# Kernel optimization log

Hardware: AMD Instinct MI355X
Metric: run time of the kernel (lower is better)

Reference implementation:

```python
import jax, jax.numpy as jnp
import numpy as np

N_OBJECTS = 32  # mask labels 1..32 (0 = background)


def setup_inputs() -> dict:
    key = jax.random.key(0)
    k1, k2, k3, k4 = jax.random.split(key, 4)
    B, F, H, W = 8, 64, 256, 256
    encoded = jax.random.normal(k1, (B, F, H, W), dtype=jnp.float32)
    masks = jax.random.randint(k2, (B, 1, H, W), 0, N_OBJECTS + 1, dtype=jnp.int32)
    W1 = jax.random.normal(k3, (2 * F, F // 2), dtype=jnp.float32) * 0.05
    b1 = jnp.zeros((F // 2,), dtype=jnp.float32)
    W2 = jax.random.normal(k4, (F // 2, 4), dtype=jnp.float32) * 0.05
    b2 = jnp.zeros((4,), dtype=jnp.float32)
    return {"encoded": encoded, "masks": masks, "W1": W1, "b1": b1, "W2": W2, "b2": b2}


def reference(encoded, masks, W1, b1, W2, b2):
    B, F, H, W = encoded.shape
    # --- masked per-object max-pool (segment max over pixels) ---
    enc = encoded.reshape(B, F, H * W).transpose(0, 2, 1)  # [B, HW, F]
    ids = masks.reshape(B, H * W)                          # [B, HW]
    seg_max = jax.vmap(
        lambda d, i: jax.ops.segment_max(d, i, num_segments=N_OBJECTS + 1)
    )(enc, ids)                                            # [B, N+1, F]
    vectors = seg_max[:, 1:, :]                            # [B, N, F] (skip label 0)

    # --- O(N^2) pairwise MLP: connections[b,c,j,i] = sigmoid(MLP([v_i; v_j])) ---
    N = vectors.shape[1]
    vi = jnp.broadcast_to(vectors[:, :, None, :], (B, N, N, F))  # v_i over axis 1
    vj = jnp.broadcast_to(vectors[:, None, :, :], (B, N, N, F))  # v_j over axis 2
    pairs = jnp.concatenate([vi, vj], axis=-1)                   # [B, N, N, 2F]
    h = jnp.einsum('bijd,dh->bijh', pairs, W1) + b1
    out = jax.nn.sigmoid(jnp.einsum('bijh,hc->bijc', h, W2) + b2)  # [B, Ni, Nj, C]
    connections = out.transpose(0, 3, 2, 1)                        # [B, C, Nj, Ni]
    return vectors, connections
```

## Files before the change

### kernel.cpp

```cpp
#include <hip/hip_runtime.h>
#include <math.h>

#define B_      8
#define F_      64
#define HW_     65536
#define NSEG    33
#define NOBJ    32
#define FPB     8
#define SLICES  16
#define PIXB    (HW_ / SLICES)
#define ENC_NEG_INF 0x007FFFFFu

__device__ __forceinline__ unsigned enc_f(float x) {
    unsigned u = __float_as_uint(x);
    return u ^ ((unsigned)((int)u >> 31) | 0x80000000u);
}
__device__ __forceinline__ float dec_f(unsigned e) {
    unsigned x = (e & 0x80000000u) ? (e ^ 0x80000000u) : ~e;
    return __uint_as_float(x);
}


__global__ __launch_bounds__(256) void segmax_kernel(
        const float* __restrict__ enc, const int* __restrict__ masks,
        float* __restrict__ part) {
    __shared__ unsigned acc[FPB * NSEG * 32];
    const int tid = threadIdx.x;
    const int blk = blockIdx.x;
    const int b     = blk >> 7;
    const int fg    = (blk >> 4) & 7;
    const int slice = blk & 15;

    for (int i = tid; i < FPB * NSEG * 32; i += 256) acc[i] = ENC_NEG_INF;
    __syncthreads();

    const int fl = tid >> 5;
    const int l  = tid & 31;
    unsigned* a = acc + fl * (NSEG * 32) + l;

    const float4* ep = (const float4*)(enc + ((size_t)(b * F_ + fg * FPB + fl)) * HW_
                                       + slice * PIXB) + l;
    const int4*   mp = (const int4*)(masks + (size_t)b * HW_ + slice * PIXB) + l;

    #pragma unroll 8
    for (int c = 0; c < PIXB / 128; ++c) {
        float4 v  = ep[c * 32];
        int4   id = mp[c * 32];
        atomicMax(a + id.x * 32, enc_f(v.x));
        atomicMax(a + id.y * 32, enc_f(v.y));
        atomicMax(a + id.z * 32, enc_f(v.z));
        atomicMax(a + id.w * 32, enc_f(v.w));
    }
    __syncthreads();

    float* dst = part + (((size_t)b * SLICES + slice) * NSEG) * F_;
    for (int cell = tid; cell < FPB * NSEG; cell += 256) {
        int f = cell & 7, s = cell >> 3;
        const unsigned* row = acc + f * (NSEG * 32) + s * 32;
        unsigned m = ENC_NEG_INF;
        #pragma unroll
        for (int k = 0; k < 32; k += 4) {
            uint4 q = *(const uint4*)(row + k);
            unsigned m1 = q.x > q.y ? q.x : q.y;
            unsigned m2 = q.z > q.w ? q.z : q.w;
            unsigned m3 = m1 > m2 ? m1 : m2;
            m = m > m3 ? m : m3;
        }
        dst[s * F_ + fg * FPB + f] = dec_f(m);
    }
}

__global__ __launch_bounds__(256) void mlp_kernel(
        const float* __restrict__ part,
        const float* __restrict__ W1, const float* __restrict__ b1,
        const float* __restrict__ W2, const float* __restrict__ b2,
        float* __restrict__ out_vec, float* __restrict__ out_conn) {
    const int b   = blockIdx.x >> 2;
    const int it  = blockIdx.x & 3;
    const int tid = threadIdx.x;
    __shared__ float v[NOBJ * 65];
    __shared__ float w1s[2 * F_ * 32];
    __shared__ float w2s[32 * 4];
    __shared__ float b1s[32];
    __shared__ float Am[8 * 36];
    __shared__ float Bm[NOBJ * 36];

    for (int i = tid; i < 2 * F_ * 32 / 4; i += 256)
        ((float4*)w1s)[i] = ((const float4*)W1)[i];
    if (tid < 32) { w2s[tid*4+0]=W2[tid*4+0]; w2s[tid*4+1]=W2[tid*4+1];
                    w2s[tid*4+2]=W2[tid*4+2]; w2s[tid*4+3]=W2[tid*4+3];
                    b1s[tid] = b1[tid]; }

    for (int cell = tid; cell < NOBJ * F_; cell += 256) {
        int s = (cell >> 6) + 1, f = cell & 63;
        float m = -INFINITY;
        #pragma unroll
        for (int sl = 0; sl < SLICES; ++sl)
            m = fmaxf(m, part[(((size_t)b * SLICES + sl) * NSEG + s) * F_ + f]);
        v[(s - 1) * 65 + f] = m;
        if (it == 0) out_vec[b * NOBJ * F_ + cell] = m;
    }
    __syncthreads();

    for (int d = tid; d < 320; d += 256) {
        int kg, obj, half;
        if (d < 64) { half = 0; obj = it * 8 + (d >> 3); kg = d & 7; }
        else        { half = 1; obj = (d - 64) >> 3;     kg = d & 7; }
        const float* vv = v + obj * 65;
        const float* w  = w1s + half * (F_ * 32) + kg * 4;
        float4 s4 = {0.f, 0.f, 0.f, 0.f};
        #pragma unroll
        for (int f = 0; f < F_; ++f) {
            float4 wf = *(const float4*)(w + f * 32);
            float x = vv[f];
            s4.x = fmaf(x, wf.x, s4.x); s4.y = fmaf(x, wf.y, s4.y);
            s4.z = fmaf(x, wf.z, s4.z); s4.w = fmaf(x, wf.w, s4.w);
        }
        if (half == 0) {
            float4 bb = *(const float4*)(b1s + kg * 4);
            s4.x += bb.x; s4.y += bb.y; s4.z += bb.z; s4.w += bb.w;
            *(float4*)(Am + (d >> 3) * 36 + kg * 4) = s4;
        } else {
            *(float4*)(Bm + obj * 36 + kg * 4) = s4;
        }
    }
    __syncthreads();

    {
        int i_loc = tid >> 5, j = tid & 31;
        float o0 = b2[0], o1 = b2[1], o2 = b2[2], o3 = b2[3];
        #pragma unroll
        for (int kg = 0; kg < 8; ++kg) {
            float4 ha = *(const float4*)(Am + i_loc * 36 + kg * 4);
            float4 hb = *(const float4*)(Bm + j * 36 + kg * 4);
            float h0 = ha.x + hb.x, h1 = ha.y + hb.y;
            float h2 = ha.z + hb.z, h3 = ha.w + hb.w;
            const float* w2 = w2s + kg * 16;
            o0 = fmaf(h0, w2[0],  fmaf(h1, w2[4],  fmaf(h2, w2[8],  fmaf(h3, w2[12], o0))));
            o1 = fmaf(h0, w2[1],  fmaf(h1, w2[5],  fmaf(h2, w2[9],  fmaf(h3, w2[13], o1))));
            o2 = fmaf(h0, w2[2],  fmaf(h1, w2[6],  fmaf(h2, w2[10], fmaf(h3, w2[14], o2))));
            o3 = fmaf(h0, w2[3],  fmaf(h1, w2[7],  fmaf(h2, w2[11], fmaf(h3, w2[15], o3))));
        }
        float* oc = out_conn + (size_t)b * 4 * NOBJ * NOBJ + j * NOBJ + (it * 8 + i_loc);
        oc[0 * NOBJ * NOBJ] = 1.f / (1.f + expf(-o0));
        oc[1 * NOBJ * NOBJ] = 1.f / (1.f + expf(-o1));
        oc[2 * NOBJ * NOBJ] = 1.f / (1.f + expf(-o2));
        oc[3 * NOBJ * NOBJ] = 1.f / (1.f + expf(-o3));
    }
}

extern "C" void kernel_launch(void* const* d_in, const int* in_sizes, int n_in,
                              void* d_out, int out_size, void* d_ws, size_t ws_size,
                              hipStream_t stream) {
    const float* enc   = (const float*)d_in[0];
    const int*   masks = (const int*)  d_in[1];
    const float* W1    = (const float*)d_in[2];
    const float* b1    = (const float*)d_in[3];
    const float* W2    = (const float*)d_in[4];
    const float* b2    = (const float*)d_in[5];

    float* out_vec  = (float*)d_out;
    float* out_conn = out_vec + B_ * NOBJ * F_;
    float* part     = (float*)d_ws;

    segmax_kernel<<<B_ * (F_ / FPB) * SLICES, 256, 0, stream>>>(enc, masks, part);
    mlp_kernel<<<B_ * 4, 256, 0, stream>>>(part, W1, b1, W2, b2, out_vec, out_conn);
}
```

Baseline: 217.1 us.

## Merge slice partials via global atomicMax and batch loads before LDS atomics

Instead of writing 16 per-slice partial maxima and reducing them in the MLP kernel, each segmax block folds its result into a pre-initialised global buffer with a guarded atomicMax, and the MLP kernel just decodes one value per cell. The segment-0 background row is no longer reduced or stored. The main loop now issues 8 vector loads before the LDS atomics so more memory requests are in flight, and the launch bounds ask for 4 blocks per CU. This adds a third small kernel launch for initialisation and global atomic traffic, in exchange for removing the partial-buffer reduction and giving the load-bound pixel loop more memory-level parallelism.

```diff
diff --git a/kernel.cpp b/kernel.cpp
--- a/kernel.cpp
+++ b/kernel.cpp
@@ -7,6 +7,7 @@
 #define NSEG    33
 #define NOBJ    32
 #define FPB     8
+#define FGRP    (F_ / FPB)
 #define SLICES  16
 #define PIXB    (HW_ / SLICES)
 #define ENC_NEG_INF 0x007FFFFFu
@@ -20,16 +21,18 @@
     return __uint_as_float(x);
 }
 
+__global__ void init_ws(unsigned* __restrict__ gws) {
+    gws[blockIdx.x * blockDim.x + threadIdx.x] = ENC_NEG_INF;
+}
 
-__global__ __launch_bounds__(256) void segmax_kernel(
+__global__ __launch_bounds__(256, 4) void segmax_kernel(
         const float* __restrict__ enc, const int* __restrict__ masks,
-        float* __restrict__ part) {
+        unsigned* __restrict__ gws) {
     __shared__ unsigned acc[FPB * NSEG * 32];
-    const int tid = threadIdx.x;
-    const int blk = blockIdx.x;
-    const int b     = blk >> 7;
-    const int fg    = (blk >> 4) & 7;
-    const int slice = blk & 15;
+    const int tid   = threadIdx.x;
+    const int b     = blockIdx.x >> 7;
+    const int fg    = (blockIdx.x >> 4) & 7;
+    const int slice = blockIdx.x & 15;
 
     for (int i = tid; i < FPB * NSEG * 32; i += 256) acc[i] = ENC_NEG_INF;
     __syncthreads();
@@ -42,36 +45,41 @@
                                        + slice * PIXB) + l;
     const int4*   mp = (const int4*)(masks + (size_t)b * HW_ + slice * PIXB) + l;
 
-    #pragma unroll 8
-    for (int c = 0; c < PIXB / 128; ++c) {
-        float4 v  = ep[c * 32];
-        int4   id = mp[c * 32];
-        atomicMax(a + id.x * 32, enc_f(v.x));
-        atomicMax(a + id.y * 32, enc_f(v.y));
-        atomicMax(a + id.z * 32, enc_f(v.z));
-        atomicMax(a + id.w * 32, enc_f(v.w));
+    for (int t = 0; t < 4; ++t) {
+        float4 v[8]; int4 id[8];
+        #pragma unroll
+        for (int u = 0; u < 8; ++u) {
+            v[u]  = ep[(t * 8 + u) * 32];
+            id[u] = mp[(t * 8 + u) * 32];
+        }
+        #pragma unroll
+        for (int u = 0; u < 8; ++u) {
+            atomicMax(a + id[u].x * 32, enc_f(v[u].x));
+            atomicMax(a + id[u].y * 32, enc_f(v[u].y));
+            atomicMax(a + id[u].z * 32, enc_f(v[u].z));
+            atomicMax(a + id[u].w * 32, enc_f(v[u].w));
+        }
     }
     __syncthreads();
 
-    float* dst = part + (((size_t)b * SLICES + slice) * NSEG) * F_;
-    for (int cell = tid; cell < FPB * NSEG; cell += 256) {
-        int f = cell & 7, s = cell >> 3;
-        const unsigned* row = acc + f * (NSEG * 32) + s * 32;
-        unsigned m = ENC_NEG_INF;
-        #pragma unroll
-        for (int k = 0; k < 32; k += 4) {
-            uint4 q = *(const uint4*)(row + k);
-            unsigned m1 = q.x > q.y ? q.x : q.y;
-            unsigned m2 = q.z > q.w ? q.z : q.w;
-            unsigned m3 = m1 > m2 ? m1 : m2;
-            m = m > m3 ? m : m3;
-        }
-        dst[s * F_ + fg * FPB + f] = dec_f(m);
+    const int fl2 = tid >> 5;
+    const int s   = (tid & 31) + 1;
+    const unsigned* row = acc + fl2 * (NSEG * 32) + s * 32;
+    unsigned m = ENC_NEG_INF;
+    #pragma unroll
+    for (int k = 0; k < 32; k += 4) {
+        uint4 q = *(const uint4*)(row + k);
+        unsigned m1 = q.x > q.y ? q.x : q.y;
+        unsigned m2 = q.z > q.w ? q.z : q.w;
+        unsigned m3 = m1 > m2 ? m1 : m2;
+        m = m > m3 ? m : m3;
     }
+    unsigned* gb = gws + b * (NOBJ * F_) + (s - 1) * F_ + (fg * FPB + fl2);
+    if (m > *gb) atomicMax(gb, m);
 }
 
 __global__ __launch_bounds__(256) void mlp_kernel(
-        const float* __restrict__ part,
+        const unsigned* __restrict__ gws,
         const float* __restrict__ W1, const float* __restrict__ b1,
         const float* __restrict__ W2, const float* __restrict__ b2,
         float* __restrict__ out_vec, float* __restrict__ out_conn) {
@@ -92,13 +100,9 @@
                     b1s[tid] = b1[tid]; }
 
     for (int cell = tid; cell < NOBJ * F_; cell += 256) {
-        int s = (cell >> 6) + 1, f = cell & 63;
-        float m = -INFINITY;
-        #pragma unroll
-        for (int sl = 0; sl < SLICES; ++sl)
-            m = fmaxf(m, part[(((size_t)b * SLICES + sl) * NSEG + s) * F_ + f]);
-        v[(s - 1) * 65 + f] = m;
-        if (it == 0) out_vec[b * NOBJ * F_ + cell] = m;
+        float m = dec_f(gws[b * (NOBJ * F_) + cell]);
+        v[(cell >> 6) * 65 + (cell & 63)] = m;
+        if (it == 0) out_vec[b * (NOBJ * F_) + cell] = m;
     }
     __syncthreads();
 
@@ -161,8 +165,9 @@
 
     float* out_vec  = (float*)d_out;
     float* out_conn = out_vec + B_ * NOBJ * F_;
-    float* part     = (float*)d_ws;
+    unsigned* gws   = (unsigned*)d_ws;
 
-    segmax_kernel<<<B_ * (F_ / FPB) * SLICES, 256, 0, stream>>>(enc, masks, part);
-    mlp_kernel<<<B_ * 4, 256, 0, stream>>>(part, W1, b1, W2, b2, out_vec, out_conn);
+    init_ws<<<B_ * NOBJ * F_ / 256, 256, 0, stream>>>(gws);
+    segmax_kernel<<<B_ * FGRP * SLICES, 256, 0, stream>>>(enc, masks, gws);
+    mlp_kernel<<<B_ * 4, 256, 0, stream>>>(gws, W1, b1, W2, b2, out_vec, out_conn);
 }
```

New measurement: 223.4 us. 2.9% more time.
